# Kernel tuning notes

Measured on AMD Instinct MI355X. Metric: run time of the kernel, lower is better.

## Reference

```python
import jax, jax.numpy as jnp
import numpy as np

B, T, D, H = 16, 2048, 1024, 64  # batch, seq_len(block_sz), emb_dim, head_sz


def setup_inputs() -> dict:
    key = jax.random.key(0)
    k0, k1, k2, k3 = jax.random.split(key, 4)
    x = jax.random.normal(k0, (B, T, D), dtype=jnp.float32)
    # nn.Linear(D, H, bias=False) weights, stored as [D, H] so y = x @ W
    s = 1.0 / np.sqrt(D)
    Wq = jax.random.uniform(k1, (D, H), dtype=jnp.float32, minval=-s, maxval=s)
    Wk = jax.random.uniform(k2, (D, H), dtype=jnp.float32, minval=-s, maxval=s)
    Wv = jax.random.uniform(k3, (D, H), dtype=jnp.float32, minval=-s, maxval=s)
    return {"x": x, "Wq": Wq, "Wk": Wk, "Wv": Wv}


def reference(x, Wq, Wk, Wv):
    # Single-head causal self-attention, naive (materializes full [B,T,T] scores).
    q = x @ Wq  # [B, T, H]
    k = x @ Wk  # [B, T, H]
    v = x @ Wv  # [B, T, H]
    scale = 1.0 / (q.shape[-1] ** 0.5)
    w = jnp.einsum("btd,bsd->bts", q, k) * scale  # [B, T, T]
    causal = jnp.tril(jnp.ones((T, T), dtype=bool))
    w = jnp.where(causal, w, -jnp.inf)
    w = jax.nn.softmax(w, axis=-1)
    # dropout p=0.0 -> identity
    out = jnp.einsum("bts,bsd->btd", w, v)  # [B, T, H]
    return out
```

## Files before the change

### kernel.cpp

```cpp
#include <hip/hip_runtime.h>
#include <math.h>

#define BB 16
#define TT 2048
#define DD 1024
#define HH 64
#define QK_SCALE 0.18033688011112042f

typedef short bf16x8 __attribute__((ext_vector_type(8)));
typedef short bf16x4 __attribute__((ext_vector_type(4)));
typedef float f32x4 __attribute__((ext_vector_type(4)));

__device__ __forceinline__ short f2bf(float f) {
  union { float f; unsigned u; } c; c.f = f;
  unsigned u = c.u + 0x7FFFu + ((c.u >> 16) & 1u);
  return (short)(u >> 16);
}
__device__ __forceinline__ short f2bf_up(float f) {
  union { float f; unsigned u; } c; c.f = f;
  return (short)((c.u + 0x8000u) >> 16);
}

__device__ __forceinline__ void* lds_swz(void* base, int row, int col) {
  int byte = (row << 7) + (col << 1);
  byte ^= (row & 7) << 4;
  return (void*)((char*)base + byte);
}

__device__ __forceinline__ void pack16(const float4& a0, const float4& a1,
                                       const float4& a2, const float4& a3,
                                       bf16x8& s0, bf16x8& s1) {
  s0[0] = f2bf(a0.x); s0[1] = f2bf(a0.y); s0[2] = f2bf(a0.z); s0[3] = f2bf(a0.w);
  s0[4] = f2bf(a1.x); s0[5] = f2bf(a1.y); s0[6] = f2bf(a1.z); s0[7] = f2bf(a1.w);
  s1[0] = f2bf(a2.x); s1[1] = f2bf(a2.y); s1[2] = f2bf(a2.z); s1[3] = f2bf(a2.w);
  s1[4] = f2bf(a3.x); s1[5] = f2bf(a3.y); s1[6] = f2bf(a3.z); s1[7] = f2bf(a3.w);
}

__global__ __launch_bounds__(256) void pack_wt(
    const float* __restrict__ Wq, const float* __restrict__ Wk,
    const float* __restrict__ Wv, short* __restrict__ wt) {
  const int idx = blockIdx.x * 256 + threadIdx.x;
  const int n = idx >> 7;
  const int k0 = (idx & 127) << 3;
  const float* W = (n < 64) ? Wq : (n < 128) ? Wk : Wv;
  const int h = n & 63;
  bf16x8 o;
#pragma unroll
  for (int j = 0; j < 8; ++j) o[j] = f2bf(W[(k0 + j) * HH + h]);
  *(bf16x8*)&wt[n * DD + k0] = o;
}

__global__ __launch_bounds__(256) void qkv_mfma(
    const float* __restrict__ x, const short* __restrict__ wt,
    short* __restrict__ qo, short* __restrict__ ko, short* __restrict__ vt) {
  __shared__ short xs[2][64 * 64];
  const int tid = threadIdx.x;
  const int lane = tid & 63;
  const int w = tid >> 6;
  const int q16 = lane & 15;
  const int g = lane >> 4;
  const size_t r0 = (size_t)blockIdx.x * 64;

  const int srow = tid >> 2;
  const int sc = (tid & 3) << 4;
  const float* xrow = x + (r0 + srow) * DD + sc;

  f32x4 acc[4][3];
#pragma unroll
  for (int mf = 0; mf < 4; ++mf)
#pragma unroll
    for (int nf = 0; nf < 3; ++nf) acc[mf][nf] = (f32x4){0.f, 0.f, 0.f, 0.f};

  const short* wp[3];
#pragma unroll
  for (int nf = 0; nf < 3; ++nf)
    wp[nf] = wt + (size_t)(w * 48 + nf * 16 + q16) * DD + g * 8;

  float4 xa[2][4];
  {
    const float4* xp = (const float4*)xrow;
#pragma unroll
    for (int j = 0; j < 4; ++j) xa[0][j] = xp[j];
    bf16x8 s0, s1;
    pack16(xa[0][0], xa[0][1], xa[0][2], xa[0][3], s0, s1);
    *(bf16x8*)lds_swz(xs[0], srow, sc) = s0;
    *(bf16x8*)lds_swz(xs[0], srow, sc + 8) = s1;
    const float4* xp1 = (const float4*)(xrow + 64);
#pragma unroll
    for (int j = 0; j < 4; ++j) xa[1][j] = xp1[j];
  }
  bf16x8 bcur[3][2];
#pragma unroll
  for (int nf = 0; nf < 3; ++nf)
#pragma unroll
    for (int kf = 0; kf < 2; ++kf)
      bcur[nf][kf] = *(const bf16x8*)(wp[nf] + kf * 32);
  __syncthreads();

  int cur = 0;
#pragma unroll 2
  for (int ks = 0; ks < 16; ++ks) {
    const int pnext = (ks + 1) & 1;
    const int pfree = ks & 1;
    if (ks < 14) {
      const float4* xp = (const float4*)(xrow + (ks + 2) * 64);
#pragma unroll
      for (int j = 0; j < 4; ++j) xa[pfree][j] = xp[j];
    }
    bf16x8 bnxt[3][2];
    if (ks < 15) {
      const int k1 = (ks + 1) << 6;
#pragma unroll
      for (int nf = 0; nf < 3; ++nf)
#pragma unroll
        for (int kf = 0; kf < 2; ++kf)
          bnxt[nf][kf] = *(const bf16x8*)(wp[nf] + k1 + kf * 32);
    }

    bf16x8 afr[4][2];
#pragma unroll
    for (int mf = 0; mf < 4; ++mf)
#pragma unroll
      for (int kf = 0; kf < 2; ++kf)
        afr[mf][kf] = *(bf16x8*)lds_swz(xs[cur], mf * 16 + q16, kf * 32 + g * 8);

#pragma unroll
    for (int mf = 0; mf < 4; ++mf)
#pragma unroll
      for (int nf = 0; nf < 3; ++nf)
#pragma unroll
        for (int kf = 0; kf < 2; ++kf)
          acc[mf][nf] = __builtin_amdgcn_mfma_f32_16x16x32_bf16(
              afr[mf][kf], bcur[nf][kf], acc[mf][nf], 0, 0, 0);

    if (ks < 15) {
      bf16x8 s0, s1;
      pack16(xa[pnext][0], xa[pnext][1], xa[pnext][2], xa[pnext][3], s0, s1);
      *(bf16x8*)lds_swz(xs[cur ^ 1], srow, sc) = s0;
      *(bf16x8*)lds_swz(xs[cur ^ 1], srow, sc + 8) = s1;
      __syncthreads();
      cur ^= 1;
#pragma unroll
      for (int nf = 0; nf < 3; ++nf)
#pragma unroll
        for (int kf = 0; kf < 2; ++kf) bcur[nf][kf] = bnxt[nf][kf];
    }
  }

#pragma unroll
  for (int nf = 0; nf < 3; ++nf) {
    const int n = w * 48 + nf * 16 + q16;
    const int mat = n >> 6;
    const int h = n & 63;
    if (mat < 2) {
      short* outp = mat ? ko : qo;
      const float fac = mat ? 1.0f : QK_SCALE;
#pragma unroll
      for (int mf = 0; mf < 4; ++mf)
#pragma unroll
        for (int r = 0; r < 4; ++r)
          outp[(r0 + mf * 16 + g * 4 + r) * HH + h] = f2bf(acc[mf][nf][r] * fac);
    } else {
      const int bb = (int)(r0 >> 11);
      const int tloc = (int)(r0 & 2047);
#pragma unroll
      for (int mf = 0; mf < 4; ++mf) {
        bf16x4 pk;
#pragma unroll
        for (int r = 0; r < 4; ++r) pk[r] = f2bf(acc[mf][nf][r]);
        *(bf16x4*)&vt[((size_t)bb * HH + h) * TT + tloc + mf * 16 + g * 4] = pk;
      }
    }
  }
}

__global__ __launch_bounds__(256, 4) void attn_mfma(
    const short* __restrict__ q, const short* __restrict__ k,
    const short* __restrict__ vt, float* __restrict__ out) {
  __shared__ short klds[2][64 * 64];
  __shared__ short vlds[2][64 * 64];

  const int bx = blockIdx.x;
  const int b = blockIdx.y;
  const int qt = (b >= 8) ? bx : (31 - bx);
  const int t0 = qt << 6;
  const int tid = threadIdx.x;
  const int lane = tid & 63;
  const int w = tid >> 6;
  const int q16 = lane & 15;
  const int g = lane >> 4;
  const int NC = qt + 1;

  const size_t brow = (size_t)b * TT;
  const short* kg = k + brow * HH;
  const short* vtg = vt + (size_t)b * HH * TT;

  const int srow = tid >> 2;
  const int scol = (tid & 3) << 4;

  bf16x8 kr0 = *(const bf16x8*)&kg[srow * HH + scol];
  bf16x8 kr1 = *(const bf16x8*)&kg[srow * HH + scol + 8];
  bf16x8 vr0 = *(const bf16x8*)&vtg[srow * TT + scol];
  bf16x8 vr1 = *(const bf16x8*)&vtg[srow * TT + scol + 8];

  {
    const short* qsrc = q + (brow + t0 + srow) * HH;
    *(bf16x8*)lds_swz(klds[0], srow, scol) = *(const bf16x8*)&qsrc[scol];
    *(bf16x8*)lds_swz(klds[0], srow, scol + 8) = *(const bf16x8*)&qsrc[scol + 8];
  }
  __syncthreads();
  bf16x8 qa[2];
#pragma unroll
  for (int kf = 0; kf < 2; ++kf)
    qa[kf] = *(bf16x8*)lds_swz(klds[0], w * 16 + q16, kf * 32 + g * 8);
  __syncthreads();

  *(bf16x8*)lds_swz(klds[0], srow, scol) = kr0;
  *(bf16x8*)lds_swz(klds[0], srow, scol + 8) = kr1;
  *(bf16x8*)lds_swz(vlds[0], srow, scol) = vr0;
  *(bf16x8*)lds_swz(vlds[0], srow, scol + 8) = vr1;
  __syncthreads();

  f32x4 po[4];
  f32x4 lacc = (f32x4){0.f, 0.f, 0.f, 0.f};
  float m = -INFINITY;
#pragma unroll
  for (int nf = 0; nf < 4; ++nf) po[nf] = (f32x4){0.f, 0.f, 0.f, 0.f};

  const bf16x8 ones = {0x3F80, 0x3F80, 0x3F80, 0x3F80,
                       0x3F80, 0x3F80, 0x3F80, 0x3F80};
  int cur = 0;

  for (int c = 0; c < NC; ++c) {
    const bool notlast = (c + 1 < NC);
    if (notlast) {
      const int s1 = (c + 1) << 6;
      kr0 = *(const bf16x8*)&kg[(s1 + srow) * HH + scol];
      kr1 = *(const bf16x8*)&kg[(s1 + srow) * HH + scol + 8];
      vr0 = *(const bf16x8*)&vtg[srow * TT + s1 + scol];
      vr1 = *(const bf16x8*)&vtg[srow * TT + s1 + scol + 8];
    }

    f32x4 sfr[4];
#pragma unroll
    for (int nf = 0; nf < 4; ++nf) sfr[nf] = (f32x4){0.f, 0.f, 0.f, 0.f};
    __builtin_amdgcn_s_setprio(1);
#pragma unroll
    for (int nf = 0; nf < 4; ++nf)
#pragma unroll
      for (int kf = 0; kf < 2; ++kf) {
        bf16x8 kb = *(bf16x8*)lds_swz(klds[cur], nf * 16 + q16, kf * 32 + g * 8);
        sfr[nf] = __builtin_amdgcn_mfma_f32_16x16x32_bf16(kb, qa[kf], sfr[nf], 0, 0, 0);
      }
    __builtin_amdgcn_s_setprio(0);

    if (c == NC - 1) {
      const int qloc = w * 16 + q16;
#pragma unroll
      for (int nf = 0; nf < 4; ++nf)
#pragma unroll
        for (int r = 0; r < 4; ++r)
          if (16 * nf + 4 * g + r > qloc) sfr[nf][r] = -INFINITY;
    }

    float pm;
    {
      f32x4 t01 = (f32x4){fmaxf(sfr[0][0], sfr[1][0]), fmaxf(sfr[0][1], sfr[1][1]),
                          fmaxf(sfr[0][2], sfr[1][2]), fmaxf(sfr[0][3], sfr[1][3])};
      f32x4 t23 = (f32x4){fmaxf(sfr[2][0], sfr[3][0]), fmaxf(sfr[2][1], sfr[3][1]),
                          fmaxf(sfr[2][2], sfr[3][2]), fmaxf(sfr[2][3], sfr[3][3])};
      pm = fmaxf(fmaxf(fmaxf(t01[0], t23[0]), fmaxf(t01[1], t23[1])),
                 fmaxf(fmaxf(t01[2], t23[2]), fmaxf(t01[3], t23[3])));
      pm = fmaxf(pm, __shfl_xor(pm, 16));
      pm = fmaxf(pm, __shfl_xor(pm, 32));
    }

    if (__any(pm - m > 8.f)) {
      const float mn = fmaxf(m, pm);
      const float corr = exp2f(m - mn);
      m = mn;
      const int sbase = (lane & 48) + ((lane >> 4) << 2);
#pragma unroll
      for (int r = 0; r < 4; ++r) {
        const float cr = __shfl(corr, sbase + r);
        lacc[r] *= cr;
#pragma unroll
        for (int nf = 0; nf < 4; ++nf) po[nf][r] *= cr;
      }
    }

    bf16x8 pa[2];
#pragma unroll
    for (int m2 = 0; m2 < 2; ++m2)
#pragma unroll
      for (int j = 0; j < 8; ++j)
        pa[m2][j] = f2bf_up(exp2f(sfr[2 * m2 + (j >> 2)][j & 3] - m));

    __builtin_amdgcn_s_setprio(1);
#pragma unroll
    for (int m2 = 0; m2 < 2; ++m2) {
#pragma unroll
      for (int nf = 0; nf < 4; ++nf) {
        bf16x4 lo = *(bf16x4*)lds_swz(vlds[cur], nf * 16 + q16, 32 * m2 + 4 * g);
        bf16x4 hi = *(bf16x4*)lds_swz(vlds[cur], nf * 16 + q16, 32 * m2 + 16 + 4 * g);
        bf16x8 vb = __builtin_shufflevector(lo, hi, 0, 1, 2, 3, 4, 5, 6, 7);
        po[nf] = __builtin_amdgcn_mfma_f32_16x16x32_bf16(pa[m2], vb, po[nf], 0, 0, 0);
      }
      lacc = __builtin_amdgcn_mfma_f32_16x16x32_bf16(pa[m2], ones, lacc, 0, 0, 0);
    }
    __builtin_amdgcn_s_setprio(0);

    if (notlast) {
      *(bf16x8*)lds_swz(klds[cur ^ 1], srow, scol) = kr0;
      *(bf16x8*)lds_swz(klds[cur ^ 1], srow, scol + 8) = kr1;
      *(bf16x8*)lds_swz(vlds[cur ^ 1], srow, scol) = vr0;
      *(bf16x8*)lds_swz(vlds[cur ^ 1], srow, scol + 8) = vr1;
      __syncthreads();
      cur ^= 1;
    }
  }

  const int qrow = t0 + w * 16 + g * 4;
#pragma unroll
  for (int nf = 0; nf < 4; ++nf) {
    const int h = nf * 16 + q16;
#pragma unroll
    for (int r = 0; r < 4; ++r)
      out[(brow + qrow + r) * HH + h] = po[nf][r] / lacc[r];
  }
}

extern "C" void kernel_launch(void* const* d_in, const int* in_sizes, int n_in,
                              void* d_out, int out_size, void* d_ws, size_t ws_size,
                              hipStream_t stream) {
  const float* x  = (const float*)d_in[0];
  const float* Wq = (const float*)d_in[1];
  const float* Wk = (const float*)d_in[2];
  const float* Wv = (const float*)d_in[3];
  float* out = (float*)d_out;

  const size_t bth = (size_t)BB * TT * HH;
  short* qb  = (short*)d_ws;
  short* kb  = qb + bth;
  short* vtb = kb + bth;
  short* wtb = vtb + bth;

  pack_wt<<<96, 256, 0, stream>>>(Wq, Wk, Wv, wtb);
  qkv_mfma<<<(BB * TT) / 64, 256, 0, stream>>>(x, wtb, qb, kb, vtb);
  attn_mfma<<<dim3(32, BB), 256, 0, stream>>>(qb, kb, vtb, out);
}
```

Measured before the change: 80.64 us.

## Permute V tile on load for single LDS read and reorder block schedule

V^T rows are now fetched as 4-element pieces and permuted while staging into LDS, so the PV loop reads one 8-element vector per MFMA operand instead of two 4-element reads plus a shuffle. The grid becomes 1-D with a mapping that puts the longest causal tiles of all batches first, then the short ones, which should balance the load across CUs. The cost is twice as many smaller global loads for V, which may coalesce worse.

Result: no change. 80.38 us (-0.3%).

```diff
diff --git a/kernel.cpp b/kernel.cpp
--- a/kernel.cpp
+++ b/kernel.cpp
@@ -180,9 +180,10 @@
   __shared__ short klds[2][64 * 64];
   __shared__ short vlds[2][64 * 64];
 
-  const int bx = blockIdx.x;
-  const int b = blockIdx.y;
-  const int qt = (b >= 8) ? bx : (31 - bx);
+  const int id = blockIdx.x;
+  const int b = (id & 7) | (((id >> 3) & 1) << 3);
+  const int kk = id >> 4;
+  const int qt = (kk < 16) ? (31 - kk) : (kk - 16);
   const int t0 = qt << 6;
   const int tid = threadIdx.x;
   const int lane = tid & 63;
@@ -198,10 +199,17 @@
   const int srow = tid >> 2;
   const int scol = (tid & 3) << 4;
 
+  const int vgA = (scol >> 3) & 3;
+  const int vgB = ((scol + 8) >> 3) & 3;
+  const int vm2 = scol >> 5;
+  const short* vrow_p = vtg + srow * TT + vm2 * 32;
+
   bf16x8 kr0 = *(const bf16x8*)&kg[srow * HH + scol];
   bf16x8 kr1 = *(const bf16x8*)&kg[srow * HH + scol + 8];
-  bf16x8 vr0 = *(const bf16x8*)&vtg[srow * TT + scol];
-  bf16x8 vr1 = *(const bf16x8*)&vtg[srow * TT + scol + 8];
+  bf16x4 va0 = *(const bf16x4*)(vrow_p + 4 * vgA);
+  bf16x4 va1 = *(const bf16x4*)(vrow_p + 16 + 4 * vgA);
+  bf16x4 vb0 = *(const bf16x4*)(vrow_p + 4 * vgB);
+  bf16x4 vb1 = *(const bf16x4*)(vrow_p + 16 + 4 * vgB);
 
   {
     const short* qsrc = q + (brow + t0 + srow) * HH;
@@ -217,8 +225,10 @@
 
   *(bf16x8*)lds_swz(klds[0], srow, scol) = kr0;
   *(bf16x8*)lds_swz(klds[0], srow, scol + 8) = kr1;
-  *(bf16x8*)lds_swz(vlds[0], srow, scol) = vr0;
-  *(bf16x8*)lds_swz(vlds[0], srow, scol + 8) = vr1;
+  *(bf16x8*)lds_swz(vlds[0], srow, scol) =
+      __builtin_shufflevector(va0, va1, 0, 1, 2, 3, 4, 5, 6, 7);
+  *(bf16x8*)lds_swz(vlds[0], srow, scol + 8) =
+      __builtin_shufflevector(vb0, vb1, 0, 1, 2, 3, 4, 5, 6, 7);
   __syncthreads();
 
   f32x4 po[4];
@@ -237,8 +247,10 @@
       const int s1 = (c + 1) << 6;
       kr0 = *(const bf16x8*)&kg[(s1 + srow) * HH + scol];
       kr1 = *(const bf16x8*)&kg[(s1 + srow) * HH + scol + 8];
-      vr0 = *(const bf16x8*)&vtg[srow * TT + s1 + scol];
-      vr1 = *(const bf16x8*)&vtg[srow * TT + s1 + scol + 8];
+      va0 = *(const bf16x4*)(vrow_p + s1 + 4 * vgA);
+      va1 = *(const bf16x4*)(vrow_p + s1 + 16 + 4 * vgA);
+      vb0 = *(const bf16x4*)(vrow_p + s1 + 4 * vgB);
+      vb1 = *(const bf16x4*)(vrow_p + s1 + 16 + 4 * vgB);
     }
 
     f32x4 sfr[4];
@@ -301,9 +313,7 @@
     for (int m2 = 0; m2 < 2; ++m2) {
 #pragma unroll
       for (int nf = 0; nf < 4; ++nf) {
-        bf16x4 lo = *(bf16x4*)lds_swz(vlds[cur], nf * 16 + q16, 32 * m2 + 4 * g);
-        bf16x4 hi = *(bf16x4*)lds_swz(vlds[cur], nf * 16 + q16, 32 * m2 + 16 + 4 * g);
-        bf16x8 vb = __builtin_shufflevector(lo, hi, 0, 1, 2, 3, 4, 5, 6, 7);
+        bf16x8 vb = *(bf16x8*)lds_swz(vlds[cur], nf * 16 + q16, m2 * 32 + g * 8);
         po[nf] = __builtin_amdgcn_mfma_f32_16x16x32_bf16(pa[m2], vb, po[nf], 0, 0, 0);
       }
       lacc = __builtin_amdgcn_mfma_f32_16x16x32_bf16(pa[m2], ones, lacc, 0, 0, 0);
@@ -313,8 +323,10 @@
     if (notlast) {
       *(bf16x8*)lds_swz(klds[cur ^ 1], srow, scol) = kr0;
       *(bf16x8*)lds_swz(klds[cur ^ 1], srow, scol + 8) = kr1;
-      *(bf16x8*)lds_swz(vlds[cur ^ 1], srow, scol) = vr0;
-      *(bf16x8*)lds_swz(vlds[cur ^ 1], srow, scol + 8) = vr1;
+      *(bf16x8*)lds_swz(vlds[cur ^ 1], srow, scol) =
+          __builtin_shufflevector(va0, va1, 0, 1, 2, 3, 4, 5, 6, 7);
+      *(bf16x8*)lds_swz(vlds[cur ^ 1], srow, scol + 8) =
+          __builtin_shufflevector(vb0, vb1, 0, 1, 2, 3, 4, 5, 6, 7);
       __syncthreads();
       cur ^= 1;
     }
@@ -347,5 +359,5 @@
 
   pack_wt<<<96, 256, 0, stream>>>(Wq, Wk, Wv, wtb);
   qkv_mfma<<<(BB * TT) / 64, 256, 0, stream>>>(x, wtb, qb, kb, vtb);
-  attn_mfma<<<dim3(32, BB), 256, 0, stream>>>(qb, kb, vtb, out);
-}
+  attn_mfma<<<512, 256, 0, stream>>>(qb, kb, vtb, out);
+}
```
